# Performance work log

Measured on AMD Instinct MI355X. Metric: run time of the kernel, lower is better.

The kernel has to match this reference:

```python
import jax, jax.numpy as jnp
import numpy as np

NUM_GROUPS = 32
EPS = 1e-5


def group_norm(x, scale, bias):
    # x: [b, c, h, w]
    b, c, h, w = x.shape
    xg = x.reshape(b, NUM_GROUPS, c // NUM_GROUPS, h, w)
    mean = jnp.mean(xg, axis=(2, 3, 4), keepdims=True)
    var = jnp.var(xg, axis=(2, 3, 4), keepdims=True)
    xg = (xg - mean) * jax.lax.rsqrt(var + EPS)
    xn = xg.reshape(b, c, h, w)
    return xn * scale[None, :, None, None] + bias[None, :, None, None]


def conv1x1(x, w, b):
    # x: [b, c_in, h, w], w: [c_out, c_in], b: [c_out]
    return jnp.einsum('bchw,dc->bdhw', x, w) + b[None, :, None, None]


def setup_inputs() -> dict:
    key = jax.random.key(0)
    ks = jax.random.split(key, 11)
    B, C, H, W = 16, 512, 32, 32
    s = 1.0 / np.sqrt(C)
    inp = {
        'x': jax.random.normal(ks[0], (B, C, H, W), jnp.float32),
        'gn_scale': jnp.ones((C,), jnp.float32),
        'gn_bias': jnp.zeros((C,), jnp.float32),
        'wq': jax.random.normal(ks[1], (C, C), jnp.float32) * s,
        'bq': jnp.zeros((C,), jnp.float32),
        'wk': jax.random.normal(ks[2], (C, C), jnp.float32) * s,
        'bk': jnp.zeros((C,), jnp.float32),
        'wv': jax.random.normal(ks[3], (C, C), jnp.float32) * s,
        'bv': jnp.zeros((C,), jnp.float32),
        'wp': jax.random.normal(ks[4], (C, C), jnp.float32) * s,
        'bp': jnp.zeros((C,), jnp.float32),
    }
    return inp


def reference(x, gn_scale, gn_bias, wq, bq, wk, bk, wv, bv, wp, bp):
    b, c, h, w = x.shape
    xn = group_norm(x, gn_scale, gn_bias)
    q = conv1x1(xn, wq, bq).reshape(b, c, h * w)  # [b, c, n]
    k = conv1x1(xn, wk, bk).reshape(b, c, h * w)
    v = conv1x1(xn, wv, bv).reshape(b, c, h * w)
    # attn[b, i, j] = sum_c q[b, c, i] * k[b, c, j]
    attn = jnp.einsum('bci,bcj->bij', q, k) * (c ** -0.5)
    A = jax.nn.softmax(attn, axis=-1)
    # out[b, c, i] = sum_j A[b, i, j] * v[b, c, j]
    out = jnp.einsum('bij,bcj->bci', A, v).reshape(b, c, h, w)
    scores = conv1x1(out, wp, bp)
    return x + scores
```

## Files before the change

kernel.cpp:

```cpp
#include <hip/hip_runtime.h>

typedef __bf16 bf16x8 __attribute__((ext_vector_type(8)));
typedef float  f32x4  __attribute__((ext_vector_type(4)));

__device__ __forceinline__ unsigned short f2bf(float f) {
    union { float f; unsigned int u; } x; x.f = f;
    unsigned int r = (x.u + 0x7FFFu + ((x.u >> 16) & 1u)) >> 16;
    return (unsigned short)r;
}

typedef const __attribute__((address_space(1))) unsigned short gu16;
typedef __attribute__((address_space(3)))       unsigned short lu16;
__device__ __forceinline__ void gl_lds16(const unsigned short* g, unsigned short* l) {
    __builtin_amdgcn_global_load_lds((gu16*)g, (lu16*)l, 16, 0, 0);
}


__device__ __forceinline__ void stageB23(
    const unsigned short* __restrict__ Bb, int ldb,
    unsigned short* LB, int t, int buf, int wave, int lane)
{
    const int kc = t * 64 + (((lane & 7) ^ ((lane >> 3) & 7)) << 3);
    unsigned short* dst = LB + buf * 24576 + 8192 + wave * 512;
    const int R = wave * 8 + (lane >> 3);
    gl_lds16(Bb + (long)R * ldb + kc,         dst);
    gl_lds16(Bb + (long)(R + 64) * ldb + kc,  dst + 4096);
    gl_lds16(Bb + (long)(R + 128) * ldb + kc, dst + 8192);
    gl_lds16(Bb + (long)(R + 192) * ldb + kc, dst + 12288);
}
__device__ __forceinline__ void stageA23(
    const unsigned short* __restrict__ Ab, int lda,
    unsigned short* LB, int t, int buf, int wave, int lane)
{
    const int kc = t * 64 + (((lane & 7) ^ ((lane >> 3) & 7)) << 3);
    unsigned short* dst = LB + buf * 24576 + wave * 512;
    const int R = wave * 8 + (lane >> 3);
    gl_lds16(Ab + (long)R * lda + kc,        dst);
    gl_lds16(Ab + (long)(R + 64) * lda + kc, dst + 4096);
}

template<int NT>
__device__ __forceinline__ void gemm23_core(
    const unsigned short* __restrict__ Ab, int lda,
    const unsigned short* __restrict__ Bb, int ldb,
    f32x4 (&acc)[4][4], unsigned short* LB)
{
    const int tid  = threadIdx.x;
    const int lane = tid & 63;
    const int wave = tid >> 6;
    const int wM   = wave >> 2;
    const int wN   = wave & 3;
    const int l16  = lane & 15;
    const int quad = lane >> 4;
    const int ck   = quad ^ (l16 & 7);
    const int aoff = (wM * 64 + l16) * 64;
    const int boff = 8192 + (wN * 64 + l16) * 64;

    stageB23(Bb, ldb, LB, 0, 0, wave, lane);
    stageA23(Ab, lda, LB, 0, 0, wave, lane);
    stageB23(Bb, ldb, LB, 1, 1, wave, lane);
    stageA23(Ab, lda, LB, 1, 1, wave, lane);
    asm volatile("s_waitcnt vmcnt(6)" ::: "memory");
    __builtin_amdgcn_s_barrier();
    __builtin_amdgcn_sched_barrier(0);

    bf16x8 af[4][2], bf[4][2];

#define RD_ALL(buf)                                                           \
    _Pragma("unroll")                                                         \
    for (int n = 0; n < 4; ++n)                                               \
        _Pragma("unroll")                                                     \
        for (int kk = 0; kk < 2; ++kk)                                        \
            bf[n][kk] = *(const bf16x8*)&LB[(buf) * 24576 + boff + n * 1024 + ((ck ^ (kk << 2)) << 3)]; \
    _Pragma("unroll")                                                         \
    for (int m = 0; m < 4; ++m)                                               \
        _Pragma("unroll")                                                     \
        for (int kk = 0; kk < 2; ++kk)                                        \
            af[m][kk] = *(const bf16x8*)&LB[(buf) * 24576 + aoff + m * 1024 + ((ck ^ (kk << 2)) << 3)];
#define MF32                                                                  \
    __builtin_amdgcn_s_setprio(1);                                            \
    _Pragma("unroll")                                                         \
    for (int m = 0; m < 4; ++m)                                               \
        _Pragma("unroll")                                                     \
        for (int n = 0; n < 4; ++n)                                           \
            _Pragma("unroll")                                                 \
            for (int kk = 0; kk < 2; ++kk)                                    \
                acc[m][n] = __builtin_amdgcn_mfma_f32_16x16x32_bf16(          \
                    af[m][kk], bf[n][kk], acc[m][n], 0, 0, 0);                \
    __builtin_amdgcn_s_setprio(0);

    int b = 0, b2 = 2;
    for (int t = 0; t < NT; ++t) {
        RD_ALL(b)
        if (t + 2 < NT) {
            stageB23(Bb, ldb, LB, t + 2, b2, wave, lane);
            stageA23(Ab, lda, LB, t + 2, b2, wave, lane);
        }
        __builtin_amdgcn_s_barrier();
        __builtin_amdgcn_sched_barrier(0);
        asm volatile("s_waitcnt lgkmcnt(0)" ::: "memory");
        __builtin_amdgcn_sched_barrier(0);
        MF32
        if (t + 2 < NT) { asm volatile("s_waitcnt vmcnt(6)" ::: "memory"); }
        else            { asm volatile("s_waitcnt vmcnt(0)" ::: "memory"); }
        __builtin_amdgcn_s_barrier();
        __builtin_amdgcn_sched_barrier(0);
        b  = (b == 2)  ? 0 : b + 1;
        b2 = (b2 == 2) ? 0 : b2 + 1;
    }
#undef RD_ALL
#undef MF32
}

template<int NT, int BMH>
__device__ __forceinline__ void stage8g(
    const unsigned short* __restrict__ Ab, int lda,
    const unsigned short* __restrict__ Bb, int ldb,
    unsigned short* LB, int s, int wave, int lane)
{
    if (s >= 4 * NT) return;
    const int tau  = s >> 2;
    const int pi   = s & 3;
    const int half = pi & 1;
    const int kc   = tau * 64 + (((lane & 7) ^ ((lane >> 3) & 7)) << 3);
    if (pi >= 2) {
        unsigned short* dst = LB + (tau & 1) * (BMH * 8192) + half * (BMH * 4096) + wave * 512;
        const int R = half * (BMH * 64) + wave * 8 + (lane >> 3);
        gl_lds16(Ab + (long)R * lda + kc, dst);
        if constexpr (BMH == 2) gl_lds16(Ab + (long)(R + 64) * lda + kc, dst + 4096);
    } else {
        unsigned short* dst = LB + (BMH * 16384) + (tau & 1) * 16384 + half * 8192 + wave * 512;
        const int R = half * 128 + wave * 8 + (lane >> 3);
        gl_lds16(Bb + (long)R * ldb + kc, dst);
        gl_lds16(Bb + (long)(R + 64) * ldb + kc, dst + 4096);
    }
}

template<int NT, int BMH>
__device__ __forceinline__ void gemm8_core(
    const unsigned short* __restrict__ Ab, int lda,
    const unsigned short* __restrict__ Bb, int ldb,
    f32x4 (&acc)[4 * BMH][4], unsigned short* LB)
{
    const int tid  = threadIdx.x;
    const int lane = tid & 63;
    const int wave = tid >> 6;
    const int wM   = wave >> 2;
    const int wN   = wave & 3;
    const int l16  = lane & 15;
    const int quad = lane >> 4;
    const int ck   = quad ^ (l16 & 7);
    const int aoff = wM * (BMH * 4096) + l16 * 64;
    const int boff = BMH * 16384 + (wN >> 1) * 8192 + ((wN & 1) * 64 + l16) * 64;

#define VMW do { if constexpr (BMH == 2) asm volatile("s_waitcnt vmcnt(6)" ::: "memory"); \
                 else                    asm volatile("s_waitcnt vmcnt(5)" ::: "memory"); } while (0)

    #pragma unroll
    for (int s = 0; s < 7; ++s)
        stage8g<NT, BMH>(Ab, lda, Bb, ldb, LB, s, wave, lane);
    VMW;
    __builtin_amdgcn_s_barrier();
    __builtin_amdgcn_sched_barrier(0);

    bf16x8 af[2 * BMH][2], bf[4][2];

#define RD_A(buf, mh)                                                         \
    _Pragma("unroll")                                                         \
    for (int m = 0; m < 2 * BMH; ++m)                                         \
        _Pragma("unroll")                                                     \
        for (int kk = 0; kk < 2; ++kk)                                        \
            af[m][kk] = *(const bf16x8*)&LB[(buf) * (BMH * 8192) + aoff + ((mh) * 2 * BMH + m) * 1024 + ((ck ^ (kk << 2)) << 3)];
#define RD_B(buf)                                                             \
    _Pragma("unroll")                                                         \
    for (int n = 0; n < 4; ++n)                                               \
        _Pragma("unroll")                                                     \
        for (int kk = 0; kk < 2; ++kk)                                        \
            bf[n][kk] = *(const bf16x8*)&LB[(buf) * 16384 + boff + n * 1024 + ((ck ^ (kk << 2)) << 3)];
#define MF(mh, nh)                                                            \
    __builtin_amdgcn_s_setprio(1);                                            \
    _Pragma("unroll")                                                         \
    for (int m = 0; m < 2 * BMH; ++m)                                         \
        _Pragma("unroll")                                                     \
        for (int n = 0; n < 2; ++n)                                           \
            _Pragma("unroll")                                                 \
            for (int kk = 0; kk < 2; ++kk)                                    \
                acc[(mh) * 2 * BMH + m][(nh) * 2 + n] = __builtin_amdgcn_mfma_f32_16x16x32_bf16( \
                    af[m][kk], bf[(nh) * 2 + n][kk], acc[(mh) * 2 * BMH + m][(nh) * 2 + n], 0, 0, 0); \
    __builtin_amdgcn_s_setprio(0);
#define BARS do { __builtin_amdgcn_s_barrier(); __builtin_amdgcn_sched_barrier(0); } while (0)
#define LGW  do { asm volatile("s_waitcnt lgkmcnt(0)" ::: "memory"); __builtin_amdgcn_sched_barrier(0); } while (0)

    const int NITER = NT / 2;
    for (int i = 0; i < NITER; ++i) {
        const int s0 = 6 + 8 * i;
        RD_B(0) RD_A(0, 0)
        stage8g<NT, BMH>(Ab, lda, Bb, ldb, LB, s0 + 1, wave, lane);
        BARS; LGW;
        MF(0, 0)
        BARS;
        stage8g<NT, BMH>(Ab, lda, Bb, ldb, LB, s0 + 2, wave, lane);
        BARS;
        MF(0, 1)
        BARS;
        RD_A(0, 1)
        stage8g<NT, BMH>(Ab, lda, Bb, ldb, LB, s0 + 3, wave, lane);
        BARS; LGW;
        MF(1, 0)
        BARS;
        stage8g<NT, BMH>(Ab, lda, Bb, ldb, LB, s0 + 4, wave, lane);
        BARS;
        MF(1, 1)
        if (i == NITER - 1) { asm volatile("s_waitcnt vmcnt(0)" ::: "memory"); }
        else                { VMW; }
        BARS;
        RD_B(1) RD_A(1, 0)
        stage8g<NT, BMH>(Ab, lda, Bb, ldb, LB, s0 + 5, wave, lane);
        BARS; LGW;
        MF(0, 0)
        BARS;
        stage8g<NT, BMH>(Ab, lda, Bb, ldb, LB, s0 + 6, wave, lane);
        BARS;
        MF(0, 1)
        BARS;
        RD_A(1, 1)
        stage8g<NT, BMH>(Ab, lda, Bb, ldb, LB, s0 + 7, wave, lane);
        BARS; LGW;
        MF(1, 0)
        BARS;
        stage8g<NT, BMH>(Ab, lda, Bb, ldb, LB, s0 + 8, wave, lane);
        BARS;
        MF(1, 1)
        if (i < NITER - 1) { VMW; }
        BARS;
    }
#undef RD_A
#undef RD_B
#undef MF
#undef BARS
#undef LGW
#undef VMW
}

__global__ __launch_bounds__(512, 2) void p8_k(
    const unsigned short* __restrict__ qT,
    const unsigned short* __restrict__ kT,
    unsigned short* __restrict__ Sb,
    float* __restrict__ lsum,
    float alpha)
{
    __shared__ __align__(16) unsigned short LB[65536];
    const int z = blockIdx.z;
    const unsigned short* Ab = qT + (long)z * 524288 + (long)(blockIdx.y * 256) * 512;
    const unsigned short* Bb = kT + (long)z * 524288 + (long)(blockIdx.x * 256) * 512;
    f32x4 acc[8][4] = {};
    gemm8_core<8, 2>(Ab, 512, Bb, 512, acc, LB);

    const int lane = threadIdx.x & 63, wave = threadIdx.x >> 6;
    const int wM = wave >> 2, wN = wave & 3;
    const int l16 = lane & 15, quad = lane >> 4;
    const int gm0 = blockIdx.y * 256 + wM * 128;
    const int gn0 = blockIdx.x * 256 + wN * 64;
    unsigned short* scr = LB + wave * 8192;

    float rs[8][4];
    #pragma unroll
    for (int mi = 0; mi < 8; ++mi) { rs[mi][0] = rs[mi][1] = rs[mi][2] = rs[mi][3] = 0.f; }
    #pragma unroll
    for (int mi = 0; mi < 8; ++mi)
        #pragma unroll
        for (int ni = 0; ni < 4; ++ni) {
            f32x4 v = acc[mi][ni];
            #pragma unroll
            for (int r = 0; r < 4; ++r) {
                float e = __expf(v[r] * alpha);
                rs[mi][r] += e;
                const int row = mi * 16 + quad * 4 + r;
                const int col = ni * 16 + l16;
                scr[row * 64 + (((col >> 3) ^ (row & 7)) << 3) + (col & 7)] = f2bf(e);
            }
        }
    #pragma unroll
    for (int mi = 0; mi < 8; ++mi)
        #pragma unroll
        for (int r = 0; r < 4; ++r) {
            float s = rs[mi][r];
            s += __shfl_xor(s, 1); s += __shfl_xor(s, 2);
            s += __shfl_xor(s, 4); s += __shfl_xor(s, 8);
            if (l16 == 0)
                atomicAdd(&lsum[(long)z * 1024 + gm0 + mi * 16 + quad * 4 + r], s);
        }
    unsigned short* dst = Sb + (long)z * 1048576;
    #pragma unroll
    for (int it = 0; it < 16; ++it) {
        const int row = it * 8 + (lane >> 3);
        const int ck2 = lane & 7;
        uint4 vv = *(uint4*)&scr[row * 64 + ((ck2 ^ (row & 7)) << 3)];
        *(uint4*)&dst[(long)(gm0 + row) * 1024 + gn0 + ck2 * 8] = vv;
    }
}

__global__ __launch_bounds__(512, 2) void qkv8_k(
    const unsigned short* __restrict__ Wqkv,
    const unsigned short* __restrict__ xnT,
    unsigned short* __restrict__ qT,
    unsigned short* __restrict__ kT,
    unsigned short* __restrict__ vB,
    const float* __restrict__ bqkv)
{
    __shared__ __align__(16) unsigned short LB[73728];
    const int z = blockIdx.z;
    const unsigned short* Ab = Wqkv + (long)(blockIdx.y * 128) * 512;
    const unsigned short* Bb = xnT + (long)z * 524288 + (long)(blockIdx.x * 256) * 512;
    f32x4 acc[4][4] = {};
    gemm23_core<8>(Ab, 512, Bb, 512, acc, LB);

    const int lane = threadIdx.x & 63, wave = threadIdx.x >> 6;
    const int wM = wave >> 2, wN = wave & 3;
    const int l16 = lane & 15, quad = lane >> 4;
    const int gm0 = blockIdx.y * 128 + wM * 64;
    const int gn0 = blockIdx.x * 256 + wN * 64;
    const int mat = blockIdx.y >> 2;
    const int ml0 = gm0 & 511;
    const long zb = (long)z * 524288;
    unsigned short* scr = LB + wave * 4096;

    if (mat == 2) {
        #pragma unroll
        for (int mi = 0; mi < 4; ++mi)
            #pragma unroll
            for (int ni = 0; ni < 4; ++ni) {
                f32x4 v = acc[mi][ni];
                #pragma unroll
                for (int r = 0; r < 4; ++r) {
                    const int ml = mi * 16 + quad * 4 + r;
                    const int nc = ni * 2 + (l16 >> 3);
                    scr[ml * 64 + ((nc ^ (ml & 7)) * 8) + (l16 & 7)] = f2bf(v[r] + bqkv[gm0 + ml]);
                }
            }
        __builtin_amdgcn_s_barrier();
        const int ch2 = lane & 7, rr = lane >> 3;
        unsigned short* dst = vB + zb + gn0 + ch2 * 8;
        #pragma unroll
        for (int it = 0; it < 8; ++it) {
            const int ml = rr + it * 8;
            uint4 vv = *(uint4*)&scr[ml * 64 + ((ch2 ^ (ml & 7)) * 8)];
            *(uint4*)(dst + (long)(ml0 + ml) * 1024) = vv;
        }
    } else {
        unsigned short* dstm = (mat == 0) ? qT : kT;
        #pragma unroll
        for (int mi = 0; mi < 4; ++mi)
            #pragma unroll
            for (int ni = 0; ni < 4; ++ni) {
                f32x4 v = acc[mi][ni];
                const int nl = ni * 16 + l16;
                const int ch = mi * 2 + (quad >> 1);
                const int m4 = gm0 + mi * 16 + quad * 4;
                ushort4 p;
                p.x = f2bf(v[0] + bqkv[m4 + 0]);
                p.y = f2bf(v[1] + bqkv[m4 + 1]);
                p.z = f2bf(v[2] + bqkv[m4 + 2]);
                p.w = f2bf(v[3] + bqkv[m4 + 3]);
                *(ushort4*)&scr[nl * 64 + ((ch ^ (nl & 7)) * 8) + (quad & 1) * 4] = p;
            }
        __builtin_amdgcn_s_barrier();
        const int ch2 = lane & 7, rr = lane >> 3;
        unsigned short* dst = dstm + zb + ml0 + ch2 * 8;
        #pragma unroll
        for (int it = 0; it < 8; ++it) {
            const int nl = rr + it * 8;
            uint4 vv = *(uint4*)&scr[nl * 64 + ((ch2 ^ (nl & 7)) * 8)];
            *(uint4*)(dst + (long)(gn0 + nl) * 512) = vv;
        }
    }
}

__global__ __launch_bounds__(512, 2) void av8_k(
    const unsigned short* __restrict__ vB,
    const unsigned short* __restrict__ Sb,
    unsigned short* __restrict__ OT,
    const float* __restrict__ Lb)
{
    __shared__ __align__(16) unsigned short LB[73728];
    const int z = blockIdx.z;
    const unsigned short* Ab = vB + (long)z * 524288 + (long)(blockIdx.y * 128) * 1024;
    const unsigned short* Bb = Sb + (long)z * 1048576 + (long)(blockIdx.x * 256) * 1024;
    f32x4 acc[4][4] = {};
    gemm23_core<16>(Ab, 1024, Bb, 1024, acc, LB);

    const int lane = threadIdx.x & 63, wave = threadIdx.x >> 6;
    const int wM = wave >> 2, wN = wave & 3;
    const int l16 = lane & 15, quad = lane >> 4;
    const int gm0 = blockIdx.y * 128 + wM * 64;
    const int gn0 = blockIdx.x * 256 + wN * 64;
    unsigned short* scr = LB + wave * 4096;

    #pragma unroll
    for (int mi = 0; mi < 4; ++mi)
        #pragma unroll
        for (int ni = 0; ni < 4; ++ni) {
            f32x4 v = acc[mi][ni];
            const float invl = 1.f / Lb[(long)z * 1024 + gn0 + ni * 16 + l16];
            const int nl = ni * 16 + l16;
            const int ch = mi * 2 + (quad >> 1);
            ushort4 p;
            p.x = f2bf(v[0] * invl); p.y = f2bf(v[1] * invl);
            p.z = f2bf(v[2] * invl); p.w = f2bf(v[3] * invl);
            *(ushort4*)&scr[nl * 64 + ((ch ^ (nl & 7)) * 8) + (quad & 1) * 4] = p;
        }
    __builtin_amdgcn_s_barrier();
    const int ch2 = lane & 7, rr = lane >> 3;
    unsigned short* dst = OT + (long)z * 524288 + gm0 + ch2 * 8;
    #pragma unroll
    for (int it = 0; it < 8; ++it) {
        const int nl = rr + it * 8;
        uint4 vv = *(uint4*)&scr[nl * 64 + ((ch2 ^ (nl & 7)) * 8)];
        *(uint4*)(dst + (long)(gn0 + nl) * 512) = vv;
    }
}

__device__ __forceinline__ void stage_tiles(
    const unsigned short* __restrict__ Ab, int lda,
    const unsigned short* __restrict__ Bb, int ldb,
    int k0, unsigned short* Ad, unsigned short* Bd,
    int wave, int r0, int c0)
{
    gl_lds16(Ab + (long)r0 * lda + c0 + k0,        Ad + wave * 512);
    gl_lds16(Ab + (long)(r0 + 64) * lda + c0 + k0, Ad + 2048 + wave * 512);
    gl_lds16(Bb + (long)r0 * ldb + c0 + k0,        Bd + wave * 512);
    gl_lds16(Bb + (long)(r0 + 64) * ldb + c0 + k0, Bd + 2048 + wave * 512);
}

__device__ __forceinline__ void gemm_core_db(
    const unsigned short* __restrict__ Ab, int lda,
    const unsigned short* __restrict__ Bb, int ldb,
    int K, f32x4 (&acc)[4][4],
    unsigned short* As, unsigned short* Bs)
{
    const int tid  = threadIdx.x;
    const int lane = tid & 63;
    const int wave = tid >> 6;
    const int wm   = (wave >> 1) * 64;
    const int wn   = (wave & 1) * 64;
    const int l16  = lane & 15;
    const int quad = lane >> 4;

    const int r0 = wave * 16 + (lane >> 2);
    const int c0 = ((lane & 3) ^ ((lane >> 3) & 3)) * 8;

    stage_tiles(Ab, lda, Bb, ldb, 0, As, Bs, wave, r0, c0);

    const int sw8 = ((l16 >> 1) & 3) * 8;

    int sel = 0;
    for (int k0 = 0; k0 < K; k0 += 32) {
        __syncthreads();
        if (k0 + 32 < K)
            stage_tiles(Ab, lda, Bb, ldb, k0 + 32,
                        As + (sel ^ 1) * 4096, Bs + (sel ^ 1) * 4096, wave, r0, c0);

        const unsigned short* Ap = As + sel * 4096;
        const unsigned short* Bp = Bs + sel * 4096;
        bf16x8 af[4], bfr[4];
        #pragma unroll
        for (int mi = 0; mi < 4; mi++)
            af[mi] = *(const bf16x8*)&Ap[(wm + mi * 16 + l16) * 32 + ((quad * 8) ^ sw8)];
        #pragma unroll
        for (int ni = 0; ni < 4; ni++)
            bfr[ni] = *(const bf16x8*)&Bp[(wn + ni * 16 + l16) * 32 + ((quad * 8) ^ sw8)];
        #pragma unroll
        for (int mi = 0; mi < 4; mi++)
            #pragma unroll
            for (int ni = 0; ni < 4; ni++)
                acc[mi][ni] = __builtin_amdgcn_mfma_f32_16x16x32_bf16(af[mi], bfr[ni], acc[mi][ni], 0, 0, 0);
        sel ^= 1;
    }
}

__global__ __launch_bounds__(256) void fin_k(
    const unsigned short* __restrict__ Wp,
    const unsigned short* __restrict__ OTb,
    float* __restrict__ out,
    const float* __restrict__ bias,
    const float* __restrict__ resid)
{
    __shared__ __align__(16) unsigned short LB[16384];
    unsigned short* As = LB;
    unsigned short* Bs = LB + 8192;

    const unsigned short* Ab = Wp + (long)(blockIdx.y * 128) * 512;
    const unsigned short* Bb = OTb + (long)blockIdx.z * 524288 + (long)(blockIdx.x * 128) * 512;

    f32x4 acc[4][4] = {};
    gemm_core_db(Ab, 512, Bb, 512, 512, acc, As, Bs);

    const int lane = threadIdx.x & 63;
    const int wave = threadIdx.x >> 6;
    const int l16  = lane & 15;
    const int quad = lane >> 4;
    const int mb = blockIdx.y * 128 + (wave >> 1) * 64;
    const int nb = blockIdx.x * 128 + (wave & 1) * 64;

    #pragma unroll
    for (int mi = 0; mi < 4; mi++) {
        #pragma unroll
        for (int ni = 0; ni < 4; ni++) {
            f32x4 v = acc[mi][ni];
            const int m0 = mb + mi * 16 + quad * 4;
            const int n  = nb + ni * 16 + l16;
            const long base = (long)blockIdx.z * 524288;
            #pragma unroll
            for (int r = 0; r < 4; r++) {
                float val = v[r] + bias[m0 + r] + resid[base + (long)(m0 + r) * 1024 + n];
                out[base + (long)(m0 + r) * 1024 + n] = val;
            }
        }
    }
}

__global__ __launch_bounds__(256) void gnw_k(
    const float* __restrict__ x, const float* __restrict__ gsc,
    const float* __restrict__ gbi, unsigned short* __restrict__ xnT,
    const float* __restrict__ w0, const float* __restrict__ w1,
    const float* __restrict__ w2, const float* __restrict__ w3,
    const float* __restrict__ b0, const float* __restrict__ b1,
    const float* __restrict__ b2,
    unsigned short* __restrict__ wout, float* __restrict__ bqkv,
    float* __restrict__ lsum)
{
    __shared__ __align__(16) unsigned short ln[16 * 1024];
    __shared__ float red[8];
    const int bid = blockIdx.x;
    const int tid = threadIdx.x;

    if (bid >= 512) {
        const int j = bid - 512;
        const int m = j >> 8;
        const int i = (j & 255) * 256 + tid;
        if (m == 4) {
            if (i < 384) {
                const int which = i >> 7, off = i & 127;
                const float* src = (which == 0) ? b0 : (which == 1) ? b1 : b2;
                ((float4*)bqkv)[i] = ((const float4*)src)[off];
            }
            if (i < 16384) lsum[i] = 0.f;
            return;
        }
        const float* src = (m == 0) ? w0 : (m == 1) ? w1 : (m == 2) ? w2 : w3;
        float4 v = ((const float4*)src)[i];
        ushort4 o; o.x = f2bf(v.x); o.y = f2bf(v.y); o.z = f2bf(v.z); o.w = f2bf(v.w);
        ((ushort4*)(wout + (long)m * 262144))[i] = o;
        return;
    }

    const int b = bid >> 5, g = bid & 31;
    const int lane = tid & 63, wv = tid >> 6;

    const float4* x4 = (const float4*)(x + ((long)b * 512 + g * 16) * 1024);
    float4 vals[16];
    float s = 0.f, ss = 0.f;
    #pragma unroll
    for (int i = 0; i < 16; i++) {
        float4 v = x4[tid + i * 256];
        vals[i] = v;
        s  += v.x + v.y + v.z + v.w;
        ss += v.x * v.x + v.y * v.y + v.z * v.z + v.w * v.w;
    }
    for (int o = 32; o; o >>= 1) { s += __shfl_down(s, o); ss += __shfl_down(ss, o); }
    if (lane == 0) { red[wv * 2] = s; red[wv * 2 + 1] = ss; }
    __syncthreads();
    const float S  = red[0] + red[2] + red[4] + red[6];
    const float SS = red[1] + red[3] + red[5] + red[7];
    const float mean = S * (1.f / 16384.f);
    const float var  = SS * (1.f / 16384.f) - mean * mean;
    const float inv  = rsqrtf(var + 1e-5f);

    #pragma unroll
    for (int i = 0; i < 16; i++) {
        const int idx = tid + i * 256;
        const int c   = idx >> 8;
        const float sc = gsc[g * 16 + c] * inv;
        const float bi = gbi[g * 16 + c] - mean * sc;
        float4 v = vals[i];
        ushort4 p;
        p.x = f2bf(v.x * sc + bi); p.y = f2bf(v.y * sc + bi);
        p.z = f2bf(v.z * sc + bi); p.w = f2bf(v.w * sc + bi);
        ((ushort4*)ln)[idx] = p;
    }
    __syncthreads();

    unsigned short* op = xnT + (long)b * 1024 * 512 + g * 16;
    for (int rep = 0; rep < 4; rep++) {
        const int n = rep * 256 + tid;
        union { unsigned short u[16]; uint4 v[2]; } t;
        #pragma unroll
        for (int c = 0; c < 16; c++) t.u[c] = ln[c * 1024 + n];
        *(uint4*)&op[(long)n * 512]     = t.v[0];
        *(uint4*)&op[(long)n * 512 + 8] = t.v[1];
    }
}

extern "C" void kernel_launch(void* const* d_in, const int* in_sizes, int n_in,
                              void* d_out, int out_size, void* d_ws, size_t ws_size,
                              hipStream_t stream)
{
    const float* x   = (const float*)d_in[0];
    const float* gsc = (const float*)d_in[1];
    const float* gbi = (const float*)d_in[2];
    const float* wq  = (const float*)d_in[3];
    const float* bq  = (const float*)d_in[4];
    const float* wk  = (const float*)d_in[5];
    const float* bk  = (const float*)d_in[6];
    const float* wv  = (const float*)d_in[7];
    const float* bv  = (const float*)d_in[8];
    const float* wp  = (const float*)d_in[9];
    const float* bp  = (const float*)d_in[10];
    float* out = (float*)d_out;

    char* ws = (char*)d_ws;
    unsigned short* xnT = (unsigned short*)(ws);
    unsigned short* qT  = (unsigned short*)(ws + 16777216);
    unsigned short* kT  = (unsigned short*)(ws + 33554432);
    unsigned short* vB  = (unsigned short*)(ws + 50331648);
    unsigned short* Sb  = (unsigned short*)(ws + 67108864);
    unsigned short* Wb  = (unsigned short*)(ws + 100663296);
    float*          bqkv= (float*)        (ws + 102760448);
    float*          Lb  = (float*)        (ws + 102768640);
    unsigned short* OT  = xnT;

    gnw_k<<<1792, 256, 0, stream>>>(x, gsc, gbi, xnT,
                                    wq, wk, wv, wp, bq, bk, bv, Wb, bqkv, Lb);

    qkv8_k<<<dim3(4, 12, 16), 512, 0, stream>>>(Wb, xnT, qT, kT, vB, bqkv);

    p8_k<<<dim3(4, 4, 16), 512, 0, stream>>>(qT, kT, Sb, Lb, 0.044194173824159216f);

    av8_k<<<dim3(4, 4, 16), 512, 0, stream>>>(vB, Sb, OT, Lb);

    fin_k<<<dim3(8, 4, 16), 256, 0, stream>>>(Wb + 786432, OT, out, bp, x);
}
```

Measured before the change: 218.2 us.

## Load B operand directly from global into registers, staging only A in LDS

The shared GEMM core used by the QKV and AV kernels no longer stages the B tile through LDS. Each wave now loads its B fragments straight from global memory into registers with global_load_dwordx4, double-buffered across iterations, while A keeps a three-stage async LDS pipeline. This cuts LDS traffic and the per-block LDS footprint, which could allow more resident blocks. The cost is more VGPR pressure and uncoalesced 16-byte global loads with less reuse, because waves sharing the same B columns each fetch them separately.

```diff
diff --git a/kernel.cpp b/kernel.cpp
--- a/kernel.cpp
+++ b/kernel.cpp
@@ -2,6 +2,7 @@
 
 typedef __bf16 bf16x8 __attribute__((ext_vector_type(8)));
 typedef float  f32x4  __attribute__((ext_vector_type(4)));
+typedef int    i32x4  __attribute__((ext_vector_type(4)));
 
 __device__ __forceinline__ unsigned short f2bf(float f) {
     union { float f; unsigned int u; } x; x.f = f;
@@ -15,32 +16,16 @@
     __builtin_amdgcn_global_load_lds((gu16*)g, (lu16*)l, 16, 0, 0);
 }
 
-
-__device__ __forceinline__ void stageB23(
-    const unsigned short* __restrict__ Bb, int ldb,
-    unsigned short* LB, int t, int buf, int wave, int lane)
-{
-    const int kc = t * 64 + (((lane & 7) ^ ((lane >> 3) & 7)) << 3);
-    unsigned short* dst = LB + buf * 24576 + 8192 + wave * 512;
-    const int R = wave * 8 + (lane >> 3);
-    gl_lds16(Bb + (long)R * ldb + kc,         dst);
-    gl_lds16(Bb + (long)(R + 64) * ldb + kc,  dst + 4096);
-    gl_lds16(Bb + (long)(R + 128) * ldb + kc, dst + 8192);
-    gl_lds16(Bb + (long)(R + 192) * ldb + kc, dst + 12288);
-}
-__device__ __forceinline__ void stageA23(
-    const unsigned short* __restrict__ Ab, int lda,
-    unsigned short* LB, int t, int buf, int wave, int lane)
-{
-    const int kc = t * 64 + (((lane & 7) ^ ((lane >> 3) & 7)) << 3);
-    unsigned short* dst = LB + buf * 24576 + wave * 512;
-    const int R = wave * 8 + (lane >> 3);
-    gl_lds16(Ab + (long)R * lda + kc,        dst);
-    gl_lds16(Ab + (long)(R + 64) * lda + kc, dst + 4096);
-}
+__device__ __forceinline__ void gldx4(i32x4* d, const unsigned short* p) {
+    asm volatile("global_load_dwordx4 %0, %1, off" : "=v"(*d) : "v"(p));
+}
+__device__ __forceinline__ bf16x8 asbf(i32x4 v) {
+    union { i32x4 i; bf16x8 b; } u; u.i = v; return u.b;
+}
+
 
 template<int NT>
-__device__ __forceinline__ void gemm23_core(
+__device__ __forceinline__ void gemm_bd_core(
     const unsigned short* __restrict__ Ab, int lda,
     const unsigned short* __restrict__ Bb, int ldb,
     f32x4 (&acc)[4][4], unsigned short* LB)
@@ -54,30 +39,35 @@
     const int quad = lane >> 4;
     const int ck   = quad ^ (l16 & 7);
     const int aoff = (wM * 64 + l16) * 64;
-    const int boff = 8192 + (wN * 64 + l16) * 64;
-
-    stageB23(Bb, ldb, LB, 0, 0, wave, lane);
-    stageA23(Ab, lda, LB, 0, 0, wave, lane);
-    stageB23(Bb, ldb, LB, 1, 1, wave, lane);
-    stageA23(Ab, lda, LB, 1, 1, wave, lane);
-    asm volatile("s_waitcnt vmcnt(6)" ::: "memory");
-    __builtin_amdgcn_s_barrier();
-    __builtin_amdgcn_sched_barrier(0);
-
-    bf16x8 af[4][2], bf[4][2];
-
-#define RD_ALL(buf)                                                           \
+    const unsigned short* bp = Bb + (long)(wN * 64 + l16) * ldb + quad * 8;
+    const int src_ck = ((lane & 7) ^ ((lane >> 3) & 7)) << 3;
+    const int Ra     = wave * 8 + (lane >> 3);
+
+#define ADMA(t) do { if ((t) < NT) {                                          \
+    unsigned short* d_ = LB + ((t) % 3) * 8192 + wave * 512;                  \
+    const unsigned short* s_ = Ab + (long)Ra * lda + (t) * 64 + src_ck;       \
+    gl_lds16(s_, d_);                                                         \
+    gl_lds16(s_ + (long)64 * lda, d_ + 4096);                                 \
+} } while (0)
+
+#define BLD(t, SET) do { if ((t) < NT) {                                      \
     _Pragma("unroll")                                                         \
-    for (int n = 0; n < 4; ++n)                                               \
+    for (int ni = 0; ni < 4; ++ni)                                            \
         _Pragma("unroll")                                                     \
         for (int kk = 0; kk < 2; ++kk)                                        \
-            bf[n][kk] = *(const bf16x8*)&LB[(buf) * 24576 + boff + n * 1024 + ((ck ^ (kk << 2)) << 3)]; \
+            gldx4(&SET[ni][kk], bp + ni * 16 * ldb + (t) * 64 + kk * 32);     \
+} } while (0)
+
+#define RDA(t) do {                                                           \
+    const unsigned short* Ap_ = LB + ((t) % 3) * 8192 + aoff;                 \
     _Pragma("unroll")                                                         \
     for (int m = 0; m < 4; ++m)                                               \
         _Pragma("unroll")                                                     \
         for (int kk = 0; kk < 2; ++kk)                                        \
-            af[m][kk] = *(const bf16x8*)&LB[(buf) * 24576 + aoff + m * 1024 + ((ck ^ (kk << 2)) << 3)];
-#define MF32                                                                  \
+            af[m][kk] = *(const bf16x8*)&Ap_[m * 1024 + ((ck ^ (kk << 2)) << 3)]; \
+} while (0)
+
+#define MFB(SET)                                                              \
     __builtin_amdgcn_s_setprio(1);                                            \
     _Pragma("unroll")                                                         \
     for (int m = 0; m < 4; ++m)                                               \
@@ -86,30 +76,42 @@
             _Pragma("unroll")                                                 \
             for (int kk = 0; kk < 2; ++kk)                                    \
                 acc[m][n] = __builtin_amdgcn_mfma_f32_16x16x32_bf16(          \
-                    af[m][kk], bf[n][kk], acc[m][n], 0, 0, 0);                \
+                    af[m][kk], asbf(SET[n][kk]), acc[m][n], 0, 0, 0);         \
     __builtin_amdgcn_s_setprio(0);
 
-    int b = 0, b2 = 2;
-    for (int t = 0; t < NT; ++t) {
-        RD_ALL(b)
-        if (t + 2 < NT) {
-            stageB23(Bb, ldb, LB, t + 2, b2, wave, lane);
-            stageA23(Ab, lda, LB, t + 2, b2, wave, lane);
-        }
-        __builtin_amdgcn_s_barrier();
-        __builtin_amdgcn_sched_barrier(0);
-        asm volatile("s_waitcnt lgkmcnt(0)" ::: "memory");
-        __builtin_amdgcn_sched_barrier(0);
-        MF32
-        if (t + 2 < NT) { asm volatile("s_waitcnt vmcnt(6)" ::: "memory"); }
-        else            { asm volatile("s_waitcnt vmcnt(0)" ::: "memory"); }
-        __builtin_amdgcn_s_barrier();
-        __builtin_amdgcn_sched_barrier(0);
-        b  = (b == 2)  ? 0 : b + 1;
-        b2 = (b2 == 2) ? 0 : b2 + 1;
-    }
-#undef RD_ALL
-#undef MF32
+#define ITER(t, CUR, NXT) do {                                                \
+    RDA(t);                                                                   \
+    ADMA((t) + 2);                                                            \
+    BLD((t) + 1, NXT);                                                        \
+    __builtin_amdgcn_sched_barrier(0);                                        \
+    asm volatile("s_waitcnt lgkmcnt(0)" ::: "memory");                        \
+    __builtin_amdgcn_sched_barrier(0);                                        \
+    if ((t) <= NT - 3)      { asm volatile("s_waitcnt vmcnt(10)" ::: "memory"); } \
+    else if ((t) == NT - 2) { asm volatile("s_waitcnt vmcnt(8)"  ::: "memory"); } \
+    else                    { asm volatile("s_waitcnt vmcnt(0)"  ::: "memory"); } \
+    __builtin_amdgcn_sched_barrier(0);                                        \
+    __builtin_amdgcn_s_barrier();                                             \
+    __builtin_amdgcn_sched_barrier(0);                                        \
+    MFB(CUR)                                                                  \
+} while (0)
+
+    i32x4 bs0[4][2], bs1[4][2];
+    bf16x8 af[4][2];
+
+    ADMA(0); ADMA(1); BLD(0, bs0);
+    asm volatile("s_waitcnt vmcnt(10)" ::: "memory");
+    __builtin_amdgcn_s_barrier();
+    __builtin_amdgcn_sched_barrier(0);
+
+    for (int t = 0; t < NT; t += 2) {
+        ITER(t,     bs0, bs1);
+        ITER(t + 1, bs1, bs0);
+    }
+#undef ADMA
+#undef BLD
+#undef RDA
+#undef MFB
+#undef ITER
 }
 
 template<int NT, int BMH>
@@ -308,12 +310,12 @@
     unsigned short* __restrict__ vB,
     const float* __restrict__ bqkv)
 {
-    __shared__ __align__(16) unsigned short LB[73728];
+    __shared__ __align__(16) unsigned short LB[32768];
     const int z = blockIdx.z;
     const unsigned short* Ab = Wqkv + (long)(blockIdx.y * 128) * 512;
     const unsigned short* Bb = xnT + (long)z * 524288 + (long)(blockIdx.x * 256) * 512;
     f32x4 acc[4][4] = {};
-    gemm23_core<8>(Ab, 512, Bb, 512, acc, LB);
+    gemm_bd_core<8>(Ab, 512, Bb, 512, acc, LB);
 
     const int lane = threadIdx.x & 63, wave = threadIdx.x >> 6;
     const int wM = wave >> 2, wN = wave & 3;
@@ -382,12 +384,12 @@
     unsigned short* __restrict__ OT,
     const float* __restrict__ Lb)
 {
-    __shared__ __align__(16) unsigned short LB[73728];
+    __shared__ __align__(16) unsigned short LB[32768];
     const int z = blockIdx.z;
     const unsigned short* Ab = vB + (long)z * 524288 + (long)(blockIdx.y * 128) * 1024;
     const unsigned short* Bb = Sb + (long)z * 1048576 + (long)(blockIdx.x * 256) * 1024;
     f32x4 acc[4][4] = {};
-    gemm23_core<16>(Ab, 1024, Bb, 1024, acc, LB);
+    gemm_bd_core<16>(Ab, 1024, Bb, 1024, acc, LB);
 
     const int lane = threadIdx.x & 63, wave = threadIdx.x >> 6;
     const int wM = wave >> 2, wN = wave & 3;
```

Result: slower. 255.6 us (+17.2%).

## Double-buffer MFMA register fragments and deepen LDS prefetch in shared GEMM core

Applied to the files above, without the earlier changes.

Restructures the shared bf16 GEMM main loop used by the QKV and AV kernels into a software-pipelined form. Two sets of A/B fragment registers alternate, so LDS reads for the next K-tile are issued before the MFMAs on the current tile. Global-to-LDS prefetch is three tiles ahead instead of two, and there is one barrier per iteration instead of two. This aims to hide LDS read latency and reduce synchronization stalls. In exchange it doubles fragment register use, which risks spills or lower occupancy under the 512x2 launch bounds.

```diff
diff --git a/kernel.cpp b/kernel.cpp
--- a/kernel.cpp
+++ b/kernel.cpp
@@ -40,7 +40,7 @@
 }
 
 template<int NT>
-__device__ __forceinline__ void gemm23_core(
+__device__ __forceinline__ void gemm23p_core(
     const unsigned short* __restrict__ Ab, int lda,
     const unsigned short* __restrict__ Bb, int ldb,
     f32x4 (&acc)[4][4], unsigned short* LB)
@@ -56,28 +56,23 @@
     const int aoff = (wM * 64 + l16) * 64;
     const int boff = 8192 + (wN * 64 + l16) * 64;
 
-    stageB23(Bb, ldb, LB, 0, 0, wave, lane);
-    stageA23(Ab, lda, LB, 0, 0, wave, lane);
-    stageB23(Bb, ldb, LB, 1, 1, wave, lane);
-    stageA23(Ab, lda, LB, 1, 1, wave, lane);
-    asm volatile("s_waitcnt vmcnt(6)" ::: "memory");
-    __builtin_amdgcn_s_barrier();
-    __builtin_amdgcn_sched_barrier(0);
-
-    bf16x8 af[4][2], bf[4][2];
-
-#define RD_ALL(buf)                                                           \
+    bf16x8 af0[4][2], bf0[4][2], af1[4][2], bf1[4][2];
+
+#define RDS(AF, BF, buf) do {                                                 \
+    const unsigned short* base_ = LB + (buf) * 24576;                         \
     _Pragma("unroll")                                                         \
     for (int n = 0; n < 4; ++n)                                               \
         _Pragma("unroll")                                                     \
         for (int kk = 0; kk < 2; ++kk)                                        \
-            bf[n][kk] = *(const bf16x8*)&LB[(buf) * 24576 + boff + n * 1024 + ((ck ^ (kk << 2)) << 3)]; \
+            BF[n][kk] = *(const bf16x8*)&base_[boff + n * 1024 + ((ck ^ (kk << 2)) << 3)]; \
     _Pragma("unroll")                                                         \
     for (int m = 0; m < 4; ++m)                                               \
         _Pragma("unroll")                                                     \
         for (int kk = 0; kk < 2; ++kk)                                        \
-            af[m][kk] = *(const bf16x8*)&LB[(buf) * 24576 + aoff + m * 1024 + ((ck ^ (kk << 2)) << 3)];
-#define MF32                                                                  \
+            AF[m][kk] = *(const bf16x8*)&base_[aoff + m * 1024 + ((ck ^ (kk << 2)) << 3)]; \
+} while (0)
+
+#define MFP(AF, BF)                                                           \
     __builtin_amdgcn_s_setprio(1);                                            \
     _Pragma("unroll")                                                         \
     for (int m = 0; m < 4; ++m)                                               \
@@ -86,30 +81,46 @@
             _Pragma("unroll")                                                 \
             for (int kk = 0; kk < 2; ++kk)                                    \
                 acc[m][n] = __builtin_amdgcn_mfma_f32_16x16x32_bf16(          \
-                    af[m][kk], bf[n][kk], acc[m][n], 0, 0, 0);                \
+                    AF[m][kk], BF[n][kk], acc[m][n], 0, 0, 0);                \
     __builtin_amdgcn_s_setprio(0);
 
-    int b = 0, b2 = 2;
-    for (int t = 0; t < NT; ++t) {
-        RD_ALL(b)
-        if (t + 2 < NT) {
-            stageB23(Bb, ldb, LB, t + 2, b2, wave, lane);
-            stageA23(Ab, lda, LB, t + 2, b2, wave, lane);
-        }
-        __builtin_amdgcn_s_barrier();
-        __builtin_amdgcn_sched_barrier(0);
-        asm volatile("s_waitcnt lgkmcnt(0)" ::: "memory");
-        __builtin_amdgcn_sched_barrier(0);
-        MF32
-        if (t + 2 < NT) { asm volatile("s_waitcnt vmcnt(6)" ::: "memory"); }
-        else            { asm volatile("s_waitcnt vmcnt(0)" ::: "memory"); }
-        __builtin_amdgcn_s_barrier();
-        __builtin_amdgcn_sched_barrier(0);
-        b  = (b == 2)  ? 0 : b + 1;
-        b2 = (b2 == 2) ? 0 : b2 + 1;
-    }
-#undef RD_ALL
-#undef MF32
+#define ITERP(t, CA, CB, NA, NB) do {                                         \
+    if ((t) + 1 < NT) { RDS(NA, NB, ((t) + 1) % 3); }                         \
+    if ((t) + 3 < NT) {                                                       \
+        stageB23(Bb, ldb, LB, (t) + 3, ((t) + 3) % 3, wave, lane);            \
+        stageA23(Ab, lda, LB, (t) + 3, ((t) + 3) % 3, wave, lane);            \
+    }                                                                         \
+    __builtin_amdgcn_sched_barrier(0);                                        \
+    MFP(CA, CB)                                     \
+    asm volatile("s_waitcnt lgkmcnt(0)" ::: "memory");                        \
+    __builtin_amdgcn_sched_barrier(0);                                        \
+    if ((t) + 3 < NT)      { asm volatile("s_waitcnt vmcnt(6)" ::: "memory"); } \
+    else                   { asm volatile("s_waitcnt vmcnt(0)" ::: "memory"); } \
+    __builtin_amdgcn_sched_barrier(0);                                        \
+    __builtin_amdgcn_s_barrier();                                             \
+    __builtin_amdgcn_sched_barrier(0);                                        \
+} while (0)
+
+    stageB23(Bb, ldb, LB, 0, 0, wave, lane);
+    stageA23(Ab, lda, LB, 0, 0, wave, lane);
+    stageB23(Bb, ldb, LB, 1, 1, wave, lane);
+    stageA23(Ab, lda, LB, 1, 1, wave, lane);
+    stageB23(Bb, ldb, LB, 2, 2, wave, lane);
+    stageA23(Ab, lda, LB, 2, 2, wave, lane);
+    asm volatile("s_waitcnt vmcnt(6)" ::: "memory");
+    __builtin_amdgcn_s_barrier();
+    __builtin_amdgcn_sched_barrier(0);
+    RDS(af0, bf0, 0);
+    asm volatile("s_waitcnt lgkmcnt(0)" ::: "memory");
+    __builtin_amdgcn_sched_barrier(0);
+
+    for (int t = 0; t < NT; t += 2) {
+        ITERP(t,     af0, bf0, af1, bf1);
+        ITERP(t + 1, af1, bf1, af0, bf0);
+    }
+#undef RDS
+#undef MFP
+#undef ITERP
 }
 
 template<int NT, int BMH>
@@ -313,7 +324,7 @@
     const unsigned short* Ab = Wqkv + (long)(blockIdx.y * 128) * 512;
     const unsigned short* Bb = xnT + (long)z * 524288 + (long)(blockIdx.x * 256) * 512;
     f32x4 acc[4][4] = {};
-    gemm23_core<8>(Ab, 512, Bb, 512, acc, LB);
+    gemm23p_core<8>(Ab, 512, Bb, 512, acc, LB);
 
     const int lane = threadIdx.x & 63, wave = threadIdx.x >> 6;
     const int wM = wave >> 2, wN = wave & 3;
@@ -387,7 +398,7 @@
     const unsigned short* Ab = vB + (long)z * 524288 + (long)(blockIdx.y * 128) * 1024;
     const unsigned short* Bb = Sb + (long)z * 1048576 + (long)(blockIdx.x * 256) * 1024;
     f32x4 acc[4][4] = {};
-    gemm23_core<16>(Ab, 1024, Bb, 1024, acc, LB);
+    gemm23p_core<16>(Ab, 1024, Bb, 1024, acc, LB);
 
     const int lane = threadIdx.x & 63, wave = threadIdx.x >> 6;
     const int wM = wave >> 2, wN = wave & 3;
```

Result: no change. 217.0 us (-0.5%).
